# Performance work log

Measured on AMD Instinct MI355X. Metric: run time of the kernel, lower is better.

## Reference

```python
import jax, jax.numpy as jnp
import numpy as np

N_NODES = 100000
N_EDGES = 3200000
D_IN, D_HID, D_OUT = 64, 16, 32


def setup_inputs() -> dict:
    key = jax.random.key(0)
    k1, k2, k3, k4, k5 = jax.random.split(key, 5)
    x = jax.random.normal(k1, (N_NODES, D_IN), dtype=jnp.float32)
    edge_index = jax.random.randint(k2, (2, N_EDGES), 0, N_NODES, dtype=jnp.int64)
    edge_weight = jax.random.uniform(k3, (N_EDGES,), dtype=jnp.float32)
    # Learned params (GCNConv lin has no bias; conv bias added post-aggregation)
    W_gcn = jax.random.normal(k4, (D_IN, D_HID), dtype=jnp.float32) / np.sqrt(D_IN)
    b_gcn = jnp.zeros((D_HID,), dtype=jnp.float32)
    W_out = jax.random.normal(k5, (D_HID, D_OUT), dtype=jnp.float32) / np.sqrt(D_HID)
    b_out = jnp.zeros((D_OUT,), dtype=jnp.float32)
    return {"x": x, "edge_index": edge_index, "edge_weight": edge_weight,
            "W_gcn": W_gcn, "b_gcn": b_gcn, "W_out": W_out, "b_out": b_out}


def reference(x, edge_index, edge_weight, W_gcn, b_gcn, W_out, b_out):
    N = x.shape[0]
    # --- gcn_norm with self loops (PyG defaults: add_self_loops=True, fill=1) ---
    loop = jnp.arange(N, dtype=edge_index.dtype)
    row = jnp.concatenate([edge_index[0], loop])  # source
    col = jnp.concatenate([edge_index[1], loop])  # target
    w = jnp.concatenate([edge_weight, jnp.ones((N,), dtype=x.dtype)])
    deg = jax.ops.segment_sum(w, col, num_segments=N)  # in-degree at targets
    dinv = jnp.where(deg > 0, jax.lax.rsqrt(deg), 0.0).astype(x.dtype)
    norm = dinv[row] * w * dinv[col]  # [E+N]
    # --- transform then gather / scatter-add aggregation ---
    h = x @ W_gcn                      # [N, 16]
    msg = h[row] * norm[:, None]       # [E+N, 16]
    agg = jax.ops.segment_sum(msg, col, num_segments=N) + b_gcn
    emb = jax.nn.relu(agg)
    return emb @ W_out + b_out         # [N, 32]
```

## Files before the change

kernel.cpp:

```cpp
#include <hip/hip_runtime.h>

#define D_IN  64
#define D_HID 16
#define D_OUT 32

#define CPB      64
#define CPB_SH   6
#define NB_MAX   1600
#define BINB     128
#define BAND2_SH 12
#define KB_MAX   32
#define SEG_CAP  6144

static __device__ __forceinline__ long long ntld_ll(const void* p) {
    return __builtin_nontemporal_load((const long long*)p);
}
static __device__ __forceinline__ int ntld_i(const int* p) {
    return __builtin_nontemporal_load(p);
}

__global__ __launch_bounds__(256) void k_bincount(
        const int* __restrict__ col, int* __restrict__ cntB, int E, int NB) {
    __shared__ int hist[NB_MAX];
    for (int b = threadIdx.x; b < NB; b += 256) hist[b] = 0;
    __syncthreads();
    int chunk = (E + BINB - 1) / BINB;
    int s = blockIdx.x * chunk;
    int e = min(E, s + chunk);
    for (int i = s + threadIdx.x; i < e; i += 256)
        atomicAdd(&hist[ntld_i(col + i) >> CPB_SH], 1);
    __syncthreads();
    for (int b = threadIdx.x; b < NB; b += 256)
        cntB[(size_t)b * BINB + blockIdx.x] = hist[b];
}

__global__ __launch_bounds__(BINB) void k_scanblk(int* __restrict__ cntB,
                                                  int* __restrict__ bb, int NB) {
    __shared__ int s[BINB];
    int b = blockIdx.x;
    int v = cntB[(size_t)b * BINB + threadIdx.x];
    s[threadIdx.x] = v;
    __syncthreads();
    for (int off = 1; off < BINB; off <<= 1) {
        int t = (threadIdx.x >= off) ? s[threadIdx.x - off] : 0;
        __syncthreads();
        s[threadIdx.x] += t;
        __syncthreads();
    }
    cntB[(size_t)b * BINB + threadIdx.x] = s[threadIdx.x] - v;
    if (threadIdx.x == BINB - 1) bb[b] = s[BINB - 1];
}

__global__ void k_scanbase(int* __restrict__ bb, int NB) {
    __shared__ int s[512];
    __shared__ int basev;
    if (threadIdx.x == 0) basev = 0;
    __syncthreads();
    for (int start = 0; start < NB; start += 512) {
        int idx = start + threadIdx.x;
        int v = (idx < NB) ? bb[idx] : 0;
        s[threadIdx.x] = v;
        __syncthreads();
        for (int off = 1; off < 512; off <<= 1) {
            int t = (threadIdx.x >= off) ? s[threadIdx.x - off] : 0;
            __syncthreads();
            s[threadIdx.x] += t;
            __syncthreads();
        }
        if (idx < NB) bb[idx] = basev + s[threadIdx.x] - v;
        __syncthreads();
        if (threadIdx.x == 0) basev += s[511];
        __syncthreads();
    }
    if (threadIdx.x == 0) bb[NB] = basev;
}

__global__ __launch_bounds__(256) void k_binfill(
        const int* __restrict__ ei, const float* __restrict__ w,
        const int* __restrict__ bb, const int* __restrict__ cntB,
        int2* __restrict__ binned, int E, int NB) {
    __shared__ int cur[NB_MAX];
    for (int b = threadIdx.x; b < NB; b += 256)
        cur[b] = bb[b] + cntB[(size_t)b * BINB + blockIdx.x];
    __syncthreads();
    int chunk = (E + BINB - 1) / BINB;
    int s = blockIdx.x * chunk;
    int e = min(E, s + chunk);
    for (int i = s + threadIdx.x; i < e; i += 256) {
        int r = ntld_i(ei + i);
        int c = ntld_i(ei + E + i);
        float wt = __builtin_nontemporal_load(w + i);
        int pos = atomicAdd(&cur[c >> CPB_SH], 1);
        binned[pos] = make_int2(r | ((c & (CPB - 1)) << 20), __float_as_int(wt));
    }
}

__global__ __launch_bounds__(256) void k_bandsort(
        int2* __restrict__ binned, const int* __restrict__ bb,
        int* __restrict__ bb2, float* __restrict__ dinv, int N, int kb) {
    __shared__ int2  seg[SEG_CAP];
    __shared__ float wsum[CPB];
    __shared__ int   cnt2[KB_MAX + 1];
    __shared__ int   cur2[KB_MAX];
    int b = blockIdx.x;
    int s = bb[b], e = bb[b + 1], len = e - s;
    if (threadIdx.x < CPB) wsum[threadIdx.x] = 0.f;
    if (threadIdx.x <= kb) cnt2[threadIdx.x] = 0;
    __syncthreads();

    if (len <= SEG_CAP) {
        for (int j = threadIdx.x; j < len; j += 256) {
            int2 v = binned[s + j];
            seg[j] = v;
            atomicAdd(&wsum[(v.x >> 20) & (CPB - 1)], __int_as_float(v.y));
            atomicAdd(&cnt2[(v.x & 0xFFFFF) >> BAND2_SH], 1);
        }
        __syncthreads();
        if (threadIdx.x == 0) {
            int run = s;
            for (int k = 0; k < kb; ++k) { int c = cnt2[k]; cnt2[k] = run; run += c; }
            cnt2[kb] = run;
        }
        __syncthreads();
        if (threadIdx.x < kb)  cur2[threadIdx.x] = cnt2[threadIdx.x];
        if (threadIdx.x <= kb) bb2[(size_t)b * (kb + 1) + threadIdx.x] = cnt2[threadIdx.x];
        __syncthreads();
        for (int j = threadIdx.x; j < len; j += 256) {
            int2 v = seg[j];
            int pos = atomicAdd(&cur2[(v.x & 0xFFFFF) >> BAND2_SH], 1);
            binned[pos] = v;
        }
    } else {
        for (int j = threadIdx.x; j < len; j += 256) {
            int2 v = binned[s + j];
            atomicAdd(&wsum[(v.x >> 20) & (CPB - 1)], __int_as_float(v.y));
        }
        if (threadIdx.x <= kb)
            bb2[(size_t)b * (kb + 1) + threadIdx.x] = (threadIdx.x == 0) ? s : e;
    }
    __syncthreads();
    if (threadIdx.x < CPB) {
        int n = (b << CPB_SH) + threadIdx.x;
        if (n < N) dinv[n] = rsqrtf(1.0f + wsum[threadIdx.x]);
    }
}

__global__ __launch_bounds__(256) void k_transform(
        const float4* __restrict__ x4, const float* __restrict__ Wg,
        const float* __restrict__ dinv, float* __restrict__ hs, int N) {
    __shared__ float Wl[D_IN * D_HID];
    __shared__ float xlf[16][68];
    for (int i = threadIdx.x; i < D_IN * D_HID; i += 256) Wl[i] = Wg[i];
    const int f = threadIdx.x & 15, nl = threadIdx.x >> 4;
    for (int base = blockIdx.x * 16; base < N; base += gridDim.x * 16) {
        __syncthreads();
        int n = base + nl;
        if (n < N) {
            float4 v = x4[(size_t)n * 16 + f];
            xlf[nl][f * 4 + 0] = v.x;
            xlf[nl][f * 4 + 1] = v.y;
            xlf[nl][f * 4 + 2] = v.z;
            xlf[nl][f * 4 + 3] = v.w;
        }
        __syncthreads();
        if (n < N) {
            float acc = 0.f;
#pragma unroll
            for (int k = 0; k < D_IN; ++k) acc += xlf[nl][k] * Wl[k * D_HID + f];
            hs[(size_t)n * D_HID + f] = acc * dinv[n];
        }
    }
}

__global__ __launch_bounds__(256) void k_aggout(
        const int2* __restrict__ binned, const int* __restrict__ bb2,
        const float* __restrict__ hs, const float* __restrict__ dinv,
        const float* __restrict__ bg, const float* __restrict__ Wo,
        const float* __restrict__ bo, float* __restrict__ out, int N, int kb) {
    __shared__ float acc[CPB][D_HID + 1];
    __shared__ float Wl[D_HID * D_OUT];
    __shared__ float bgl[D_HID];
    __shared__ float bol[D_OUT];
    for (int i = threadIdx.x; i < CPB * (D_HID + 1); i += 256)
        ((float*)acc)[i] = 0.f;
    for (int i = threadIdx.x; i < D_HID * D_OUT; i += 256) Wl[i] = Wo[i];
    if (threadIdx.x < D_HID) bgl[threadIdx.x] = bg[threadIdx.x];
    if (threadIdx.x < D_OUT) bol[threadIdx.x] = bo[threadIdx.x];
    __syncthreads();

    int b = blockIdx.x;
    const int f = threadIdx.x & 15;
    const int slot = threadIdx.x >> 4;
    for (int k = 0; k < kb; ++k) {
        int bs = bb2[(size_t)b * (kb + 1) + k];
        int be = bb2[(size_t)b * (kb + 1) + k + 1];
        int i = bs + slot;
        for (; i + 16 < be; i += 32) {
            long long p0 = ntld_ll(binned + i);
            long long p1 = ntld_ll(binned + i + 16);
            int r0 = (int)p0, r1 = (int)p1;
            float h0 = hs[(size_t)(r0 & 0xFFFFF) * D_HID + f];
            float h1 = hs[(size_t)(r1 & 0xFFFFF) * D_HID + f];
            atomicAdd(&acc[(r0 >> 20) & (CPB - 1)][f],
                      h0 * __int_as_float((int)(p0 >> 32)));
            atomicAdd(&acc[(r1 >> 20) & (CPB - 1)][f],
                      h1 * __int_as_float((int)(p1 >> 32)));
        }
        if (i < be) {
            long long p = ntld_ll(binned + i);
            int r = (int)p;
            float h = hs[(size_t)(r & 0xFFFFF) * D_HID + f];
            atomicAdd(&acc[(r >> 20) & (CPB - 1)][f],
                      h * __int_as_float((int)(p >> 32)));
        }
    }
    __syncthreads();

    {
        const int nl = threadIdx.x >> 4;
#pragma unroll
        for (int rep = 0; rep < CPB / 16; ++rep) {
            int cl = nl + rep * 16;
            int n = (b << CPB_SH) + cl;
            if (n < N) {
                float di = dinv[n];
                float v = di * (acc[cl][f] + hs[(size_t)n * D_HID + f]) + bgl[f];
                acc[cl][f] = fmaxf(v, 0.f);
            }
        }
    }
    __syncthreads();

    {
        const int o  = threadIdx.x & 31;
        const int n2 = threadIdx.x >> 5;
#pragma unroll
        for (int rep = 0; rep < CPB / 8; ++rep) {
            int cl = n2 + rep * 8;
            int n = (b << CPB_SH) + cl;
            if (n < N) {
                float a = bol[o];
#pragma unroll
                for (int ff = 0; ff < D_HID; ++ff)
                    a += acc[cl][ff] * Wl[ff * D_OUT + o];
                out[(size_t)n * D_OUT + o] = a;
            }
        }
    }
}

extern "C" void kernel_launch(void* const* d_in, const int* in_sizes, int n_in,
                              void* d_out, int out_size, void* d_ws, size_t ws_size,
                              hipStream_t stream) {
    const float* x  = (const float*)d_in[0];
    const int*   ei = (const int*)d_in[1];
    const float* ew = (const float*)d_in[2];
    const float* Wg = (const float*)d_in[3];
    const float* bg = (const float*)d_in[4];
    const float* Wo = (const float*)d_in[5];
    const float* bo = (const float*)d_in[6];
    float* out = (float*)d_out;

    const int N  = in_sizes[0] / D_IN;
    const int E  = in_sizes[2];
    const int NB = (N + CPB - 1) >> CPB_SH;
    const int kb = (N + (1 << BAND2_SH) - 1) >> BAND2_SH;

    float* ws   = (float*)d_ws;
    float* dinv = ws;
    int*   bb   = (int*)(ws + N);
    size_t o2   = (size_t)N + (size_t)((NB + 2) & ~1);
    int*   bb2  = (int*)(ws + o2);
    size_t o3   = o2 + (((size_t)NB * (kb + 1) + 1) & ~(size_t)1);
    int2*  binned = (int2*)(ws + o3);
    float* hs   = ws + o3 + (size_t)2 * E;
    int*   cntB = (int*)hs;

    k_bincount<<<BINB, 256, 0, stream>>>(ei + E, cntB, E, NB);
    k_scanblk <<<NB, BINB, 0, stream>>>(cntB, bb, NB);
    k_scanbase<<<1, 512, 0, stream>>>(bb, NB);
    k_binfill <<<BINB, 256, 0, stream>>>(ei, ew, bb, cntB, binned, E, NB);
    k_bandsort<<<NB, 256, 0, stream>>>(binned, bb, bb2, dinv, N, kb);
    k_transform<<<(N + 15) / 16, 256, 0, stream>>>((const float4*)x, Wg, dinv, hs, N);
    k_aggout  <<<NB, 256, 0, stream>>>(binned, bb2, hs, dinv, bg, Wo, bo, out, N, kb);
}
```

Measured before the change: 594.0 us.

## Halve column bucket size, drop per-band bounds and unroll gather eightfold

```diff
diff --git a/kernel.cpp b/kernel.cpp
--- a/kernel.cpp
+++ b/kernel.cpp
@@ -4,13 +4,13 @@
 #define D_HID 16
 #define D_OUT 32
 
-#define CPB      64
-#define CPB_SH   6
-#define NB_MAX   1600
+#define CPB      32
+#define CPB_SH   5
+#define NB_MAX   3200
 #define BINB     128
 #define BAND2_SH 12
 #define KB_MAX   32
-#define SEG_CAP  6144
+#define SEG_CAP  2048
 
 static __device__ __forceinline__ long long ntld_ll(const void* p) {
     return __builtin_nontemporal_load((const long long*)p);
@@ -97,7 +97,7 @@
 
 __global__ __launch_bounds__(256) void k_bandsort(
         int2* __restrict__ binned, const int* __restrict__ bb,
-        int* __restrict__ bb2, float* __restrict__ dinv, int N, int kb) {
+        float* __restrict__ dinv, int N, int kb) {
     __shared__ int2  seg[SEG_CAP];
     __shared__ float wsum[CPB];
     __shared__ int   cnt2[KB_MAX + 1];
@@ -122,8 +122,7 @@
             cnt2[kb] = run;
         }
         __syncthreads();
-        if (threadIdx.x < kb)  cur2[threadIdx.x] = cnt2[threadIdx.x];
-        if (threadIdx.x <= kb) bb2[(size_t)b * (kb + 1) + threadIdx.x] = cnt2[threadIdx.x];
+        if (threadIdx.x < kb) cur2[threadIdx.x] = cnt2[threadIdx.x];
         __syncthreads();
         for (int j = threadIdx.x; j < len; j += 256) {
             int2 v = seg[j];
@@ -135,8 +134,6 @@
             int2 v = binned[s + j];
             atomicAdd(&wsum[(v.x >> 20) & (CPB - 1)], __int_as_float(v.y));
         }
-        if (threadIdx.x <= kb)
-            bb2[(size_t)b * (kb + 1) + threadIdx.x] = (threadIdx.x == 0) ? s : e;
     }
     __syncthreads();
     if (threadIdx.x < CPB) {
@@ -173,10 +170,10 @@
 }
 
 __global__ __launch_bounds__(256) void k_aggout(
-        const int2* __restrict__ binned, const int* __restrict__ bb2,
+        const int2* __restrict__ binned, const int* __restrict__ bb,
         const float* __restrict__ hs, const float* __restrict__ dinv,
         const float* __restrict__ bg, const float* __restrict__ Wo,
-        const float* __restrict__ bo, float* __restrict__ out, int N, int kb) {
+        const float* __restrict__ bo, float* __restrict__ out, int N) {
     __shared__ float acc[CPB][D_HID + 1];
     __shared__ float Wl[D_HID * D_OUT];
     __shared__ float bgl[D_HID];
@@ -189,30 +186,29 @@
     __syncthreads();
 
     int b = blockIdx.x;
+    int bs = bb[b], be = bb[b + 1];
     const int f = threadIdx.x & 15;
     const int slot = threadIdx.x >> 4;
-    for (int k = 0; k < kb; ++k) {
-        int bs = bb2[(size_t)b * (kb + 1) + k];
-        int be = bb2[(size_t)b * (kb + 1) + k + 1];
-        int i = bs + slot;
-        for (; i + 16 < be; i += 32) {
-            long long p0 = ntld_ll(binned + i);
-            long long p1 = ntld_ll(binned + i + 16);
-            int r0 = (int)p0, r1 = (int)p1;
-            float h0 = hs[(size_t)(r0 & 0xFFFFF) * D_HID + f];
-            float h1 = hs[(size_t)(r1 & 0xFFFFF) * D_HID + f];
-            atomicAdd(&acc[(r0 >> 20) & (CPB - 1)][f],
-                      h0 * __int_as_float((int)(p0 >> 32)));
-            atomicAdd(&acc[(r1 >> 20) & (CPB - 1)][f],
-                      h1 * __int_as_float((int)(p1 >> 32)));
-        }
-        if (i < be) {
-            long long p = ntld_ll(binned + i);
-            int r = (int)p;
-            float h = hs[(size_t)(r & 0xFFFFF) * D_HID + f];
-            atomicAdd(&acc[(r >> 20) & (CPB - 1)][f],
-                      h * __int_as_float((int)(p >> 32)));
-        }
+    int i = bs + slot;
+    for (; i + 112 < be; i += 128) {
+        long long p[8];
+#pragma unroll
+        for (int j = 0; j < 8; ++j) p[j] = ntld_ll(binned + i + 16 * j);
+        float h[8];
+#pragma unroll
+        for (int j = 0; j < 8; ++j)
+            h[j] = hs[(size_t)((int)p[j] & 0xFFFFF) * D_HID + f];
+#pragma unroll
+        for (int j = 0; j < 8; ++j)
+            atomicAdd(&acc[((int)p[j] >> 20) & (CPB - 1)][f],
+                      h[j] * __int_as_float((int)(p[j] >> 32)));
+    }
+    for (; i < be; i += 16) {
+        long long p = ntld_ll(binned + i);
+        int r = (int)p;
+        float h = hs[(size_t)(r & 0xFFFFF) * D_HID + f];
+        atomicAdd(&acc[(r >> 20) & (CPB - 1)][f],
+                  h * __int_as_float((int)(p >> 32)));
     }
     __syncthreads();
 
@@ -270,17 +266,15 @@
     float* dinv = ws;
     int*   bb   = (int*)(ws + N);
     size_t o2   = (size_t)N + (size_t)((NB + 2) & ~1);
-    int*   bb2  = (int*)(ws + o2);
-    size_t o3   = o2 + (((size_t)NB * (kb + 1) + 1) & ~(size_t)1);
-    int2*  binned = (int2*)(ws + o3);
-    float* hs   = ws + o3 + (size_t)2 * E;
+    int2*  binned = (int2*)(ws + o2);
+    float* hs   = ws + o2 + (size_t)2 * E;
     int*   cntB = (int*)hs;
 
     k_bincount<<<BINB, 256, 0, stream>>>(ei + E, cntB, E, NB);
     k_scanblk <<<NB, BINB, 0, stream>>>(cntB, bb, NB);
     k_scanbase<<<1, 512, 0, stream>>>(bb, NB);
     k_binfill <<<BINB, 256, 0, stream>>>(ei, ew, bb, cntB, binned, E, NB);
-    k_bandsort<<<NB, 256, 0, stream>>>(binned, bb, bb2, dinv, N, kb);
+    k_bandsort<<<NB, 256, 0, stream>>>(binned, bb, dinv, N, kb);
     k_transform<<<(N + 15) / 16, 256, 0, stream>>>((const float4*)x, Wg, dinv, hs, N);
-    k_aggout  <<<NB, 256, 0, stream>>>(binned, bb2, hs, dinv, bg, Wo, bo, out, N, kb);
-}
+    k_aggout  <<<NB, 256, 0, stream>>>(binned, bb, hs, dinv, bg, Wo, bo, out, N);
+}
```

Result: no change. 588.9 us (-0.9%).
